# Optimization experiments

Hardware: AMD Instinct MI355X
Metric: run time of the kernel (lower is better)

Reference implementation:

```python
import jax, jax.numpy as jnp
import numpy as np

N = 10000      # nodes
E = 160000     # edges (before self-loops)
IN = 256
NEG_SLOPE = 0.2  # PyG GATConv default


def gat_layer(x, src, dst, W, a_src, a_dst, bias, heads, concat, n):
    # x: [n, in_dim]; W: [in_dim, heads*C]; a_src/a_dst: [heads, C]
    C = W.shape[1] // heads
    h = (x @ W).reshape(n, heads, C)                      # [n,H,C]
    es = jnp.einsum('nhc,hc->nh', h, a_src)               # [n,H]
    ed = jnp.einsum('nhc,hc->nh', h, a_dst)               # [n,H]
    e = jax.nn.leaky_relu(es[src] + ed[dst], NEG_SLOPE)   # [E,H]
    # segment softmax over destination node (every node has a self-loop)
    emax = jax.ops.segment_max(e, dst, num_segments=n)    # [n,H]
    al = jnp.exp(e - emax[dst])                           # [E,H]
    den = jax.ops.segment_sum(al, dst, num_segments=n)    # [n,H]
    al = al / den[dst]
    out = jax.ops.segment_sum(h[src] * al[:, :, None], dst, num_segments=n)  # [n,H,C]
    out = out.reshape(n, heads * C) if concat else out.mean(axis=1)
    return out + bias


def setup_inputs() -> dict:
    key = jax.random.key(0)
    ks = jax.random.split(key, 16)
    s = 0.05
    p = lambda k, shp: jax.random.normal(k, shp, dtype=jnp.float32) * s
    return {
        'x': jax.random.normal(ks[0], (N, IN), dtype=jnp.float32),
        'edge_index': jax.random.randint(ks[1], (2, E), 0, N, dtype=jnp.int64),
        'proj_w': p(ks[2], (IN, 512)), 'proj_b': jnp.zeros((512,), jnp.float32),
        'w1': p(ks[3], (512, 4 * 512)),  'as1': p(ks[4], (4, 512)), 'ad1': p(ks[5], (4, 512)),  'b1': jnp.zeros((2048,), jnp.float32),
        'w2': p(ks[6], (2048, 4 * 512)), 'as2': p(ks[7], (4, 512)), 'ad2': p(ks[8], (4, 512)),  'b2': jnp.zeros((2048,), jnp.float32),
        'w3': p(ks[9], (2048, 2 * 512)), 'as3': p(ks[10], (2, 512)), 'ad3': p(ks[11], (2, 512)), 'b3': jnp.zeros((512,), jnp.float32),
    }


def reference(x, edge_index, proj_w, proj_b, w1, as1, ad1, b1,
              w2, as2, ad2, b2, w3, as3, ad3, b3):
    n = x.shape[0]
    loops = jnp.arange(n, dtype=edge_index.dtype)
    src = jnp.concatenate([edge_index[0], loops])   # PyG add_self_loops=True
    dst = jnp.concatenate([edge_index[1], loops])
    h = x @ proj_w + proj_b                         # dropout is identity in eval
    h = gat_layer(h, src, dst, w1, as1, ad1, b1, 4, True, n)
    h = jax.nn.elu(h)
    h = gat_layer(h, src, dst, w2, as2, ad2, b2, 4, True, n)
    h = jax.nn.elu(h)
    h = gat_layer(h, src, dst, w3, as3, ad3, b3, 2, False, n)
    return h
```

## Files before the change

### kernel.cpp

```cpp
#include <hip/hip_runtime.h>
#include <hip/hip_bf16.h>
#include <math.h>

#define CDIV(a,b) (((a)+(b)-1)/(b))

typedef __bf16  bf16x8 __attribute__((ext_vector_type(8)));
typedef float   f32x4  __attribute__((ext_vector_type(4)));
typedef unsigned short u16x8 __attribute__((ext_vector_type(8)));
typedef unsigned short u16x4 __attribute__((ext_vector_type(4)));

__device__ __forceinline__ float bf2f(unsigned short u) {
    union { unsigned int i; float f; } x; x.i = ((unsigned int)u) << 16; return x.f;
}
__device__ __forceinline__ unsigned short f2bf(float f) {
    union { float f; unsigned int i; } x; x.f = f;
    unsigned int r = x.i + 0x7fff + ((x.i >> 16) & 1);
    return (unsigned short)(r >> 16);
}

__global__ void hist_kernel(const int* __restrict__ ei, int* __restrict__ deg,
                            int E, int Et) {
    int e = blockIdx.x * blockDim.x + threadIdx.x;
    if (e >= Et) return;
    int d = (e < E) ? ei[E + e] : (e - E);
    atomicAdd(&deg[d], 1);
}

__global__ void scan_kernel(const int* __restrict__ deg, int* __restrict__ off, int n) {
    __shared__ int wsum[16];
    __shared__ int carry_s;
    int t = threadIdx.x, lane = t & 63, wv = t >> 6;
    if (t == 0) carry_s = 0;
    __syncthreads();
    for (int base = 0; base < n; base += 1024) {
        int v = (base + t < n) ? deg[base + t] : 0;
        int x = v;
#pragma unroll
        for (int o = 1; o < 64; o <<= 1) {
            int y = __shfl_up(x, o);
            if (lane >= o) x += y;
        }
        if (lane == 63) wsum[wv] = x;
        __syncthreads();
        if (wv == 0 && lane < 16) {
            int s = wsum[lane];
#pragma unroll
            for (int o = 1; o < 16; o <<= 1) {
                int y = __shfl_up(s, o);
                if (lane >= o) s += y;
            }
            wsum[lane] = s;
        }
        __syncthreads();
        int wprev = (wv == 0) ? 0 : wsum[wv - 1];
        int incl = carry_s + wprev + x;
        if (base + t < n) off[base + t] = incl - v;
        __syncthreads();
        if (t == 1023) carry_s = incl;
        __syncthreads();
    }
    if (t == 0) off[n] = carry_s;
}

__global__ void scatter_kernel(const int* __restrict__ ei, const int* __restrict__ off,
                               int* __restrict__ cur, int* __restrict__ csr,
                               int E, int Et) {
    int e = blockIdx.x * blockDim.x + threadIdx.x;
    if (e >= Et) return;
    int s, d;
    if (e < E) { s = ei[e]; d = ei[E + e]; } else { s = e - E; d = s; }
    int pos = off[d] + atomicAdd(&cur[d], 1);
    csr[pos] = s;
}

__global__ void prep_t_kernel(const float* __restrict__ wa, __hip_bfloat16* __restrict__ wta,
                              const float* __restrict__ wb, __hip_bfloat16* __restrict__ wtb,
                              const float* __restrict__ wc, __hip_bfloat16* __restrict__ wtc,
                              int t0, int t1, int t2) {
    __shared__ float tile[32][33];
    int bid = blockIdx.x;
    const float* w; __hip_bfloat16* wt; int K, N, r;
    if (bid < t0)      { w = wa; wt = wta; K = 512;  N = 2048; r = bid; }
    else if (bid < t1) { w = wb; wt = wtb; K = 2048; N = 2048; r = bid - t0; }
    else               { w = wc; wt = wtc; K = 2048; N = 1024; r = bid - t1; }
    (void)t2;
    int kt = K >> 5;
    int kb = (r % kt) * 32, nb = (r / kt) * 32;
    int tx = threadIdx.x & 31, ty = threadIdx.x >> 5;
    for (int i = ty; i < 32; i += 8)
        tile[i][tx] = w[(size_t)(kb + i) * N + nb + tx];
    __syncthreads();
    for (int i = ty; i < 32; i += 8)
        wt[(size_t)(nb + i) * K + kb + tx] = __float2bfloat16(tile[tx][i]);
}

__global__ void cvt2_kernel(const float* __restrict__ a, __hip_bfloat16* __restrict__ ao,
                            int na4,
                            const float* __restrict__ b, __hip_bfloat16* __restrict__ bo,
                            int nb4) {
    int i = blockIdx.x * blockDim.x + threadIdx.x;
    const float* src; __hip_bfloat16* dst; int idx;
    if (i < na4) { src = a; dst = ao; idx = i * 4; }
    else if (i < na4 + nb4) { src = b; dst = bo; idx = (i - na4) * 4; }
    else return;
    float4 v = *(const float4*)(src + idx);
    dst[idx + 0] = __float2bfloat16(v.x);
    dst[idx + 1] = __float2bfloat16(v.y);
    dst[idx + 2] = __float2bfloat16(v.z);
    dst[idx + 3] = __float2bfloat16(v.w);
}

__global__ void beff_kernel(const float* __restrict__ pb, const float* __restrict__ w1,
                            float* __restrict__ beff, int N) {
    int j  = blockIdx.x * 256 + threadIdx.x;
    int k0 = blockIdx.y * 64;
    float s = 0.f;
#pragma unroll
    for (int k = 0; k < 64; k++)
        s = fmaf(pb[k0 + k], w1[(size_t)(k0 + k) * N + j], s);
    atomicAdd(&beff[j], s);
}

__global__ void va_kernel(const __hip_bfloat16* __restrict__ w_efft,
                          const float* __restrict__ b_eff,
                          const float* __restrict__ as1, const float* __restrict__ ad1,
                          const float* __restrict__ b1,
                          float* __restrict__ va, float* __restrict__ cvec,
                          float* __restrict__ b1s) {
    int j = blockIdx.x, t = threadIdx.x;
    if (j == 8) {
        for (int i = t; i < 2048; i += 256) b1s[i] = b_eff[i] + b1[i];
        return;
    }
    int h = j & 3;
    const float* a = ((j < 4) ? as1 : ad1) + h * 512;
    __shared__ float aLDS[512];
    __shared__ float red[256];
    for (int c = t; c < 512; c += 256) aLDS[c] = a[c];
    __syncthreads();
    float acc = 0.f;
    const unsigned short* wb = (const unsigned short*)w_efft + (size_t)h * 512 * 256 + t;
    for (int c = 0; c < 512; c++)
        acc = fmaf(aLDS[c], bf2f(wb[(size_t)c * 256]), acc);
    va[j * 256 + t] = acc;
    float cp = b_eff[h * 512 + t] * aLDS[t] + b_eff[h * 512 + 256 + t] * aLDS[256 + t];
    red[t] = cp;
    __syncthreads();
    for (int s = 128; s > 0; s >>= 1) {
        if (t < s) red[t] += red[t + s];
        __syncthreads();
    }
    if (t == 0) cvec[j] = red[0];
}

__global__ void es1_kernel(const __hip_bfloat16* __restrict__ x_bf,
                           const float* __restrict__ va, const float* __restrict__ cvec,
                           float* __restrict__ es, float* __restrict__ ed) {
    int node = blockIdx.x, l = threadIdx.x;
    u16x4 xv = *(const u16x4*)((const unsigned short*)x_bf + (size_t)node * 256 + l * 4);
    float xf[4];
#pragma unroll
    for (int k = 0; k < 4; k++) xf[k] = bf2f(xv[k]);
    float dot[8];
#pragma unroll
    for (int j = 0; j < 8; j++) {
        float4 v = *(const float4*)(va + j * 256 + l * 4);
        dot[j] = xf[0] * v.x + xf[1] * v.y + xf[2] * v.z + xf[3] * v.w;
    }
#pragma unroll
    for (int j = 0; j < 8; j++)
        for (int o = 32; o; o >>= 1) dot[j] += __shfl_down(dot[j], o);
    if (l == 0) {
#pragma unroll
        for (int h = 0; h < 4; h++) {
            es[node * 4 + h] = dot[h] + cvec[h];
            ed[node * 4 + h] = dot[4 + h] + cvec[4 + h];
        }
    }
}

__global__ __launch_bounds__(256) void agg1x_kernel(
    const __hip_bfloat16* __restrict__ x_bf, const float* __restrict__ es,
    const float* __restrict__ ed, const int* __restrict__ csr,
    const int* __restrict__ off, __hip_bfloat16* __restrict__ z)
{
    __shared__ float alds[64][4];
    __shared__ int   slds[64];
    int d = blockIdx.x, t = threadIdx.x;
    int beg = off[d], end = off[d + 1];
    float acc[4] = {0.f, 0.f, 0.f, 0.f}, den[4] = {0.f, 0.f, 0.f, 0.f};
    float edd[4];
#pragma unroll
    for (int h = 0; h < 4; h++) edd[h] = ed[d * 4 + h];
    const unsigned short* xb = (const unsigned short*)x_bf;

    for (int cb = beg; cb < end; cb += 64) {
        int cl = end - cb; if (cl > 64) cl = 64;
        int i = t >> 2, h = t & 3;
        if (i < cl) {
            int s = csr[cb + i];
            if (h == 0) slds[i] = s;
            float e = es[s * 4 + h] + edd[h];
            e = (e > 0.f) ? e : 0.2f * e;
            alds[i][h] = __expf(e);
        }
        __syncthreads();
        for (int ii = 0; ii < cl; ii++) {
            int s = slds[ii];
            float xv = bf2f(xb[(size_t)s * 256 + t]);
#pragma unroll
            for (int hh = 0; hh < 4; hh++) {
                float a = alds[ii][hh];
                den[hh] += a;
                acc[hh] = fmaf(a, xv, acc[hh]);
            }
        }
        __syncthreads();
    }
    unsigned short* zb = (unsigned short*)z + (size_t)d * 1024;
#pragma unroll
    for (int h = 0; h < 4; h++)
        zb[h * 256 + t] = f2bf(acc[h] / den[h]);
}

__device__ __forceinline__ void gload16(void* lds, const void* g) {
    __builtin_amdgcn_global_load_lds(
        (const __attribute__((address_space(1))) void*)g,
        (__attribute__((address_space(3))) void*)lds, 16, 0, 0);
}

__global__ __launch_bounds__(256) void gemm_bf16_kernel(
    const __hip_bfloat16* __restrict__ A,
    const __hip_bfloat16* __restrict__ BT,
    const float* __restrict__ bias,
    __hip_bfloat16* __restrict__ Cb,
    int M, int N, int K, int lda, int hko, int do_elu,
    int MB, int NB, int XT, int NBH)
{
    __shared__ __align__(16) __hip_bfloat16 As[128 * 32];
    __shared__ __align__(16) __hip_bfloat16 Bs[128 * 32];

    const int bid  = blockIdx.x;
    const int xcd  = bid & 7;
    const int slot = bid >> 3;
    const int per_yh = XT * NBH;
    const int yh    = slot / per_yh;
    const int rem   = slot - yh * per_yh;
    const int x_sub = rem / NBH;
    const int ys    = rem - x_sub * NBH;
    const int yb    = yh * NBH + ys;
    const int xb    = xcd * XT + x_sub;
    if (xb >= MB || yb >= NB) return;

    const int tid = threadIdx.x;
    const int m0 = xb * 128, n0 = yb * 128;
    const int w = tid >> 6, l = tid & 63;
    const int wm = (w & 1) * 64, wn = (w >> 1) * 64;
    const int lm = l & 15, lq = l >> 4;

    f32x4 acc[4][4] = {};

    const int arow = tid >> 2;
    const int acol = (tid & 3) * 8;
    const __hip_bfloat16* Ag = A + (size_t)(m0 + arow) * lda + acol + (n0 >> 9) * hko;
    const __hip_bfloat16* Bg = BT + (size_t)(n0 + arow) * K + acol;
    char* AsW = (char*)As + (w << 10);
    char* BsW = (char*)Bs + (w << 10);

    for (int k0 = 0; k0 < K; k0 += 32) {
        gload16(AsW,        Ag + k0);
        gload16(AsW + 4096, Ag + (size_t)64 * lda + k0);
        gload16(BsW,        Bg + k0);
        gload16(BsW + 4096, Bg + (size_t)64 * K + k0);
        __syncthreads();
        bf16x8 af[4], bfr[4];
#pragma unroll
        for (int i = 0; i < 4; i++)
            af[i] = *(const bf16x8*)(As + (wm + i * 16 + lm) * 32 + lq * 8);
#pragma unroll
        for (int j = 0; j < 4; j++)
            bfr[j] = *(const bf16x8*)(Bs + (wn + j * 16 + lm) * 32 + lq * 8);
#pragma unroll
        for (int i = 0; i < 4; i++)
#pragma unroll
            for (int j = 0; j < 4; j++)
                acc[i][j] = __builtin_amdgcn_mfma_f32_16x16x32_bf16(
                    af[i], bfr[j], acc[i][j], 0, 0, 0);
        __syncthreads();
    }

#pragma unroll
    for (int i = 0; i < 4; i++) {
        int rb = m0 + wm + i * 16 + lq * 4;
#pragma unroll
        for (int r = 0; r < 4; r++) {
            int row = rb + r;
            if (row >= M) continue;
#pragma unroll
            for (int j = 0; j < 4; j++) {
                int col = n0 + wn + j * 16 + lm;
                float v = acc[i][j][r];
                if (bias) v += bias[col];
                if (do_elu) v = (v > 0.f) ? v : expm1f(v);
                Cb[(size_t)row * N + col] = __float2bfloat16(v);
            }
        }
    }
}

__global__ __launch_bounds__(512, 2) void gemm256_kernel(
    const __hip_bfloat16* __restrict__ A,
    const __hip_bfloat16* __restrict__ BT,
    __hip_bfloat16* __restrict__ Cb,
    int M, int N, int K, int MT, int nfull)
{
    __shared__ __align__(16) char smem[131072];
    const int NT = K >> 6;

    const int cpx  = gridDim.x >> 3;
    const int bid  = blockIdx.x;
    const int slot = (bid & 7) * cpx + (bid >> 3);
    int mt, ntl;
    if (slot < nfull) { mt = slot % MT; ntl = slot / MT; }
    else              { ntl = nfull / MT; mt = (nfull % MT) + (slot - nfull); }
    const int m0 = mt << 8, n0 = ntl << 8;

    const int tid = threadIdx.x;
    const int w  = tid >> 6, l = tid & 63;
    const int wr = w >> 2, wc = w & 3;
    const int lm = l & 15, lq = l >> 4;

    const int srow = tid >> 3;
    const int scol = ((l & 7) << 3) ^ ((l >> 3) << 3);
    const __hip_bfloat16* As0 = A  + (size_t)(m0 + srow) * K + scol;
    const __hip_bfloat16* Bs0 = BT + (size_t)(n0 + srow) * K + scol;
    const size_t rs64  = (size_t)64  * K;
    const size_t rs128 = (size_t)128 * K;
    char* const stA = smem +          ((size_t)w << 10);
    char* const stB = smem + 65536 +  ((size_t)w << 10);

    auto STAGE_A = [&](int par, int hf, int tt) {
        char* d = stA + (((par << 1) | hf) << 14);
        const __hip_bfloat16* s = As0 + (size_t)hf * rs128 + (tt << 6);
        gload16(d,        s);
        gload16(d + 8192, s + rs64);
    };
    auto STAGE_B = [&](int par, int hf, int tt) {
        char* d = stB + (((par << 1) | hf) << 14);
        const __hip_bfloat16* s = Bs0 + (size_t)hf * rs128 + (tt << 6);
        gload16(d,        s);
        gload16(d + 8192, s + rs64);
    };

    const int roff = lm << 7;
    const int xm   = (lm & 7) << 4;
    const int off0 = (lq << 4) ^ xm;
    const int off1 = off0 ^ 64;
    const int bsel = 65536 + ((wc & 1) << 13);

    f32x4  acc[8][4] = {};
    bf16x8 af[8][2];
    bf16x8 bfr[2][2];

    STAGE_A(0, 0, 0); STAGE_A(0, 1, 0);
    STAGE_B(0, 0, 0); STAGE_B(0, 1, 0);
    STAGE_A(1, 0, 1); STAGE_A(1, 1, 1);
    asm volatile("s_waitcnt vmcnt(4)" ::: "memory");
    __builtin_amdgcn_s_barrier();

    for (int t = 0; t < NT; ++t) {
        const int par = t & 1;
        const char* aS = smem + (((par << 1) | wr)        << 14) + roff;
        const char* bS = smem + (((par << 1) | (wc >> 1)) << 14) + bsel + roff;

#pragma unroll
        for (int i = 0; i < 4; ++i) {
            af[i][0] = *(const bf16x8*)(aS + i * 2048 + off0);
            af[i][1] = *(const bf16x8*)(aS + i * 2048 + off1);
        }
#pragma unroll
        for (int j = 0; j < 2; ++j) {
            bfr[j][0] = *(const bf16x8*)(bS + j * 2048 + off0);
            bfr[j][1] = *(const bf16x8*)(bS + j * 2048 + off1);
        }
        if (t + 1 < NT) STAGE_B(par ^ 1, 0, t + 1);
        __builtin_amdgcn_s_barrier();
        asm volatile("s_waitcnt lgkmcnt(0)" ::: "memory");
        __builtin_amdgcn_sched_barrier(0);
        __builtin_amdgcn_s_setprio(1);
#pragma unroll
        for (int i = 0; i < 4; ++i)
#pragma unroll
            for (int j = 0; j < 2; ++j) {
                acc[i][j] = __builtin_amdgcn_mfma_f32_16x16x32_bf16(af[i][0], bfr[j][0], acc[i][j], 0, 0, 0);
                acc[i][j] = __builtin_amdgcn_mfma_f32_16x16x32_bf16(af[i][1], bfr[j][1], acc[i][j], 0, 0, 0);
            }
        __builtin_amdgcn_s_setprio(0);
        __builtin_amdgcn_s_barrier();

#pragma unroll
        for (int i = 4; i < 8; ++i) {
            af[i][0] = *(const bf16x8*)(aS + i * 2048 + off0);
            af[i][1] = *(const bf16x8*)(aS + i * 2048 + off1);
        }
        if (t + 1 < NT) STAGE_B(par ^ 1, 1, t + 1);
        __builtin_amdgcn_s_barrier();
        asm volatile("s_waitcnt lgkmcnt(0)" ::: "memory");
        __builtin_amdgcn_sched_barrier(0);
        __builtin_amdgcn_s_setprio(1);
#pragma unroll
        for (int i = 4; i < 8; ++i)
#pragma unroll
            for (int j = 0; j < 2; ++j) {
                acc[i][j] = __builtin_amdgcn_mfma_f32_16x16x32_bf16(af[i][0], bfr[j][0], acc[i][j], 0, 0, 0);
                acc[i][j] = __builtin_amdgcn_mfma_f32_16x16x32_bf16(af[i][1], bfr[j][1], acc[i][j], 0, 0, 0);
            }
        __builtin_amdgcn_s_setprio(0);
        __builtin_amdgcn_s_barrier();

#pragma unroll
        for (int j = 0; j < 2; ++j) {
            bfr[j][0] = *(const bf16x8*)(bS + (j + 2) * 2048 + off0);
            bfr[j][1] = *(const bf16x8*)(bS + (j + 2) * 2048 + off1);
        }
        if (t + 2 < NT) STAGE_A(par, 0, t + 2);
        __builtin_amdgcn_s_barrier();
        asm volatile("s_waitcnt lgkmcnt(0)" ::: "memory");
        __builtin_amdgcn_sched_barrier(0);
        __builtin_amdgcn_s_setprio(1);
#pragma unroll
        for (int i = 0; i < 4; ++i)
#pragma unroll
            for (int j = 0; j < 2; ++j) {
                acc[i][j + 2] = __builtin_amdgcn_mfma_f32_16x16x32_bf16(af[i][0], bfr[j][0], acc[i][j + 2], 0, 0, 0);
                acc[i][j + 2] = __builtin_amdgcn_mfma_f32_16x16x32_bf16(af[i][1], bfr[j][1], acc[i][j + 2], 0, 0, 0);
            }
        __builtin_amdgcn_s_setprio(0);
        __builtin_amdgcn_s_barrier();

        if (t + 2 < NT) STAGE_A(par, 1, t + 2);
        __builtin_amdgcn_s_barrier();
        __builtin_amdgcn_sched_barrier(0);
        __builtin_amdgcn_s_setprio(1);
#pragma unroll
        for (int i = 4; i < 8; ++i)
#pragma unroll
            for (int j = 0; j < 2; ++j) {
                acc[i][j + 2] = __builtin_amdgcn_mfma_f32_16x16x32_bf16(af[i][0], bfr[j][0], acc[i][j + 2], 0, 0, 0);
                acc[i][j + 2] = __builtin_amdgcn_mfma_f32_16x16x32_bf16(af[i][1], bfr[j][1], acc[i][j + 2], 0, 0, 0);
            }
        __builtin_amdgcn_s_setprio(0);
        if (t + 2 < NT)      { asm volatile("s_waitcnt vmcnt(4)" ::: "memory"); }
        else if (t + 1 < NT) { asm volatile("s_waitcnt vmcnt(0)" ::: "memory"); }
        __builtin_amdgcn_s_barrier();
    }

#pragma unroll
    for (int i = 0; i < 8; ++i) {
        int rb = m0 + wr * 128 + i * 16 + lq * 4;
#pragma unroll
        for (int r = 0; r < 4; ++r) {
            int row = rb + r;
            if (row >= M) continue;
#pragma unroll
            for (int j = 0; j < 4; ++j) {
                int col = n0 + wc * 64 + j * 16 + lm;
                Cb[(size_t)row * N + col] = __float2bfloat16(acc[i][j][r]);
            }
        }
    }
}

__global__ __launch_bounds__(256, 2) void gemm128_kernel(
    const __hip_bfloat16* __restrict__ A,
    const __hip_bfloat16* __restrict__ BT,
    __hip_bfloat16* __restrict__ Cb,
    int M, int N, int K, int mode, int RT)
{
    __shared__ __align__(16) char smem[65536];
    const int NT = K >> 6;

    const int cpx  = gridDim.x >> 3;
    const int bid  = blockIdx.x;
    const int slot = (bid & 7) * cpx + (bid >> 3);
    int r, c;
    if (mode == 0) { r = slot % RT; c = slot / RT; }
    else {
        if (slot < 96) { c = 12 + slot / 48; r = 32 + slot % 48; }
        else           { int u = slot - 96; c = 14 + u / 80; r = u % 80; }
    }
    const int m0 = r << 7, n0 = c << 7;

    const int tid = threadIdx.x;
    const int w = tid >> 6, l = tid & 63;
    const int wm = (w & 1) << 6, wn = (w >> 1) << 6;
    const int lm = l & 15, lq = l >> 4;

    const int srow = tid >> 3;
    const int scol = (((tid & 7) ^ ((tid >> 3) & 7)) << 3);
    const __hip_bfloat16* Ag = A  + (size_t)(m0 + srow) * K + scol;
    const __hip_bfloat16* Bg = BT + (size_t)(n0 + srow) * K + scol;
    const size_t rs32 = (size_t)32 * K;
    char* const dA = smem +         ((size_t)w << 10);
    char* const dB = smem + 16384 + ((size_t)w << 10);

    auto STAGE = [&](int par, int tt) {
        char* pa = dA + (par << 15);
        char* pb = dB + (par << 15);
        const __hip_bfloat16* sa = Ag + (tt << 6);
        const __hip_bfloat16* sb = Bg + (tt << 6);
#pragma unroll
        for (int s = 0; s < 4; ++s) {
            gload16(pa + (s << 12), sa + (size_t)s * rs32);
            gload16(pb + (s << 12), sb + (size_t)s * rs32);
        }
    };

    const int roff = lm << 7;
    const int off0 = (lq << 4) ^ ((lm & 7) << 4);
    const int off1 = off0 ^ 64;

    f32x4 acc[4][4] = {};

    STAGE(0, 0);
    asm volatile("s_waitcnt vmcnt(0)" ::: "memory");
    __builtin_amdgcn_s_barrier();

    for (int t = 0; t < NT; ++t) {
        const int par = t & 1;
        if (t + 1 < NT) STAGE(par ^ 1, t + 1);
        const char* aS = smem + (par << 15) +         wm * 128 + roff;
        const char* bS = smem + (par << 15) + 16384 + wn * 128 + roff;
        bf16x8 af[4][2], bfr[4][2];
#pragma unroll
        for (int i = 0; i < 4; ++i) {
            af[i][0]  = *(const bf16x8*)(aS + i * 2048 + off0);
            af[i][1]  = *(const bf16x8*)(aS + i * 2048 + off1);
            bfr[i][0] = *(const bf16x8*)(bS + i * 2048 + off0);
            bfr[i][1] = *(const bf16x8*)(bS + i * 2048 + off1);
        }
        asm volatile("s_waitcnt lgkmcnt(0)" ::: "memory");
        __builtin_amdgcn_sched_barrier(0);
        __builtin_amdgcn_s_setprio(1);
#pragma unroll
        for (int i = 0; i < 4; ++i)
#pragma unroll
            for (int j = 0; j < 4; ++j) {
                acc[i][j] = __builtin_amdgcn_mfma_f32_16x16x32_bf16(af[i][0], bfr[j][0], acc[i][j], 0, 0, 0);
                acc[i][j] = __builtin_amdgcn_mfma_f32_16x16x32_bf16(af[i][1], bfr[j][1], acc[i][j], 0, 0, 0);
            }
        __builtin_amdgcn_s_setprio(0);
        if (t + 1 < NT) asm volatile("s_waitcnt vmcnt(0)" ::: "memory");
        __builtin_amdgcn_s_barrier();
    }

#pragma unroll
    for (int i = 0; i < 4; ++i) {
        int rb = m0 + wm + i * 16 + lq * 4;
#pragma unroll
        for (int r2 = 0; r2 < 4; ++r2) {
            int row = rb + r2;
            if (row >= M) continue;
#pragma unroll
            for (int j = 0; j < 4; ++j) {
                int col = n0 + wn + j * 16 + lm;
                Cb[(size_t)row * N + col] = __float2bfloat16(acc[i][j][r2]);
            }
        }
    }
}

__global__ void esed_kernel(const __hip_bfloat16* __restrict__ h,
                            const float* __restrict__ a_src,
                            const float* __restrict__ a_dst,
                            float* __restrict__ es, float* __restrict__ ed, int H) {
    int nidx = blockIdx.x;
    int t = threadIdx.x;
    int head = t >> 6, lane = t & 63;
    const unsigned short* hp =
        (const unsigned short*)h + (size_t)nidx * H * 512 + head * 512 + lane * 8;
    const float* sp = a_src + head * 512 + lane * 8;
    const float* dp = a_dst + head * 512 + lane * 8;
    u16x8 hv = *(const u16x8*)hp;
    float4 s0 = *(const float4*)sp, s1 = *(const float4*)(sp + 4);
    float4 d0 = *(const float4*)dp, d1 = *(const float4*)(dp + 4);
    float hf[8];
#pragma unroll
    for (int k = 0; k < 8; k++) hf[k] = bf2f(hv[k]);
    float s = hf[0]*s0.x + hf[1]*s0.y + hf[2]*s0.z + hf[3]*s0.w
            + hf[4]*s1.x + hf[5]*s1.y + hf[6]*s1.z + hf[7]*s1.w;
    float d = hf[0]*d0.x + hf[1]*d0.y + hf[2]*d0.z + hf[3]*d0.w
            + hf[4]*d1.x + hf[5]*d1.y + hf[6]*d1.z + hf[7]*d1.w;
    for (int o = 32; o; o >>= 1) { s += __shfl_down(s, o); d += __shfl_down(d, o); }
    if (lane == 0) { es[nidx * H + head] = s; ed[nidx * H + head] = d; }
}

template<int H>
__global__ __launch_bounds__(256) void alpha_kernel(
    const float* __restrict__ es, const float* __restrict__ ed,
    const int* __restrict__ csr, const int* __restrict__ off,
    float* __restrict__ alpha, int n)
{
    int d = blockIdx.x * 4 + (threadIdx.x >> 6);
    if (d >= n) return;
    int lane = threadIdx.x & 63;
    int beg = off[d], end = off[d + 1];
    float edd[H], den[H];
#pragma unroll
    for (int h = 0; h < H; h++) { edd[h] = ed[d * H + h]; den[h] = 0.f; }
    for (int i = beg + lane; i < end; i += 64) {
        int s = csr[i];
#pragma unroll
        for (int h = 0; h < H; h++) {
            float e = es[s * H + h] + edd[h];
            e = (e > 0.f) ? e : 0.2f * e;
            den[h] += __expf(e);
        }
    }
#pragma unroll
    for (int h = 0; h < H; h++) {
        for (int o = 32; o; o >>= 1) den[h] += __shfl_down(den[h], o);
        den[h] = __shfl(den[h], 0);
        den[h] = 1.f / den[h];
    }
    for (int i = beg + lane; i < end; i += 64) {
        int s = csr[i];
#pragma unroll
        for (int h = 0; h < H; h++) {
            float e = es[s * H + h] + edd[h];
            e = (e > 0.f) ? e : 0.2f * e;
            alpha[(size_t)i * H + h] = __expf(e) * den[h];
        }
    }
}

__global__ __launch_bounds__(256) void agg2s_kernel(
    const __hip_bfloat16* __restrict__ h, const float* __restrict__ alpha,
    const int* __restrict__ csr, const int* __restrict__ off,
    const float* __restrict__ bias, __hip_bfloat16* __restrict__ outB, int n)
{
    const int bid   = blockIdx.x;
    const int slice = bid & 7;
    const int head  = slice >> 1;
    const int wvs   = (bid >> 3) * 4 + (threadIdx.x >> 6);
    const int lane  = threadIdx.x & 63;
    const int half  = lane >> 5;
    const int c0    = slice * 256 + (lane & 31) * 8;
    const unsigned short* hb = (const unsigned short*)h;
    float bv[8];
#pragma unroll
    for (int k = 0; k < 8; k++) bv[k] = bias[c0 + k];

    for (int d = wvs; d < n; d += 1024) {
        int beg = off[d], end = off[d + 1];
        float acc[8] = {0.f, 0.f, 0.f, 0.f, 0.f, 0.f, 0.f, 0.f};
        int i = beg + half;
        for (; i + 2 < end; i += 4) {
            int s0 = csr[i], s1 = csr[i + 2];
            float a0 = alpha[(size_t)i * 4 + head];
            float a1 = alpha[(size_t)(i + 2) * 4 + head];
            u16x8 v0 = *(const u16x8*)(hb + (size_t)s0 * 2048 + c0);
            u16x8 v1 = *(const u16x8*)(hb + (size_t)s1 * 2048 + c0);
#pragma unroll
            for (int k = 0; k < 8; k++) acc[k] = fmaf(a0, bf2f(v0[k]), acc[k]);
#pragma unroll
            for (int k = 0; k < 8; k++) acc[k] = fmaf(a1, bf2f(v1[k]), acc[k]);
        }
        for (; i < end; i += 2) {
            int s0 = csr[i];
            float a0 = alpha[(size_t)i * 4 + head];
            u16x8 v0 = *(const u16x8*)(hb + (size_t)s0 * 2048 + c0);
#pragma unroll
            for (int k = 0; k < 8; k++) acc[k] = fmaf(a0, bf2f(v0[k]), acc[k]);
        }
#pragma unroll
        for (int k = 0; k < 8; k++) acc[k] += __shfl_xor(acc[k], 32);
        if (half == 0) {
            u16x8 ov;
#pragma unroll
            for (int k = 0; k < 8; k++) {
                float v = acc[k] + bv[k];
                v = (v > 0.f) ? v : expm1f(v);
                ov[k] = f2bf(v);
            }
            *(u16x8*)((unsigned short*)outB + (size_t)d * 2048 + c0) = ov;
        }
    }
}

__global__ __launch_bounds__(256) void agg3s_kernel(
    const __hip_bfloat16* __restrict__ h, const float* __restrict__ alpha,
    const int* __restrict__ csr, const int* __restrict__ off,
    float* __restrict__ part, int n)
{
    const int bid   = blockIdx.x;
    const int xcd   = bid & 7;
    const int slice = xcd >> 1;
    const int head  = slice >> 1;
    const int sb    = ((bid >> 3) << 1) | (xcd & 1);
    const int wvs   = sb * 4 + (threadIdx.x >> 6);
    const int lane  = threadIdx.x & 63;
    const int half  = lane >> 5;
    const int c0    = slice * 256 + (lane & 31) * 8;
    const unsigned short* hb = (const unsigned short*)h;

    for (int d = wvs; d < n; d += 2048) {
        int beg = off[d], end = off[d + 1];
        float acc[8] = {0.f, 0.f, 0.f, 0.f, 0.f, 0.f, 0.f, 0.f};
        int i = beg + half;
        for (; i + 2 < end; i += 4) {
            int s0 = csr[i], s1 = csr[i + 2];
            float a0 = alpha[(size_t)i * 2 + head];
            float a1 = alpha[(size_t)(i + 2) * 2 + head];
            u16x8 v0 = *(const u16x8*)(hb + (size_t)s0 * 1024 + c0);
            u16x8 v1 = *(const u16x8*)(hb + (size_t)s1 * 1024 + c0);
#pragma unroll
            for (int k = 0; k < 8; k++) acc[k] = fmaf(a0, bf2f(v0[k]), acc[k]);
#pragma unroll
            for (int k = 0; k < 8; k++) acc[k] = fmaf(a1, bf2f(v1[k]), acc[k]);
        }
        for (; i < end; i += 2) {
            int s0 = csr[i];
            float a0 = alpha[(size_t)i * 2 + head];
            u16x8 v0 = *(const u16x8*)(hb + (size_t)s0 * 1024 + c0);
#pragma unroll
            for (int k = 0; k < 8; k++) acc[k] = fmaf(a0, bf2f(v0[k]), acc[k]);
        }
#pragma unroll
        for (int k = 0; k < 8; k++) acc[k] += __shfl_xor(acc[k], 32);
        if (half == 0) {
            float* pp = part + (size_t)d * 1024 + c0;
            *(float4*)pp       = make_float4(acc[0], acc[1], acc[2], acc[3]);
            *(float4*)(pp + 4) = make_float4(acc[4], acc[5], acc[6], acc[7]);
        }
    }
}

__global__ void comb3_kernel(const float* __restrict__ part,
                             const float* __restrict__ b3,
                             float* __restrict__ out, int n) {
    int idx = blockIdx.x * 256 + threadIdx.x;
    if (idx >= n * 128) return;
    int d = idx >> 7, c = (idx & 127) * 4;
    float4 p0 = *(const float4*)(part + (size_t)d * 1024 + c);
    float4 p1 = *(const float4*)(part + (size_t)d * 1024 + 512 + c);
    float4 bb = *(const float4*)(b3 + c);
    float4 o;
    o.x = 0.5f * (p0.x + p1.x) + bb.x;
    o.y = 0.5f * (p0.y + p1.y) + bb.y;
    o.z = 0.5f * (p0.z + p1.z) + bb.z;
    o.w = 0.5f * (p0.w + p1.w) + bb.w;
    *(float4*)(out + (size_t)d * 512 + c) = o;
}

extern "C" void kernel_launch(void* const* d_in, const int* in_sizes, int n_in,
                              void* d_out, int out_size, void* d_ws, size_t ws_size,
                              hipStream_t stream) {
    const float* x      = (const float*)d_in[0];
    const int*   ei     = (const int*)  d_in[1];
    const float* proj_w = (const float*)d_in[2];
    const float* proj_b = (const float*)d_in[3];
    const float* w1  = (const float*)d_in[4];
    const float* as1 = (const float*)d_in[5];
    const float* ad1 = (const float*)d_in[6];
    const float* b1  = (const float*)d_in[7];
    const float* w2  = (const float*)d_in[8];
    const float* as2 = (const float*)d_in[9];
    const float* ad2 = (const float*)d_in[10];
    const float* b2  = (const float*)d_in[11];
    const float* w3  = (const float*)d_in[12];
    const float* as3 = (const float*)d_in[13];
    const float* ad3 = (const float*)d_in[14];
    const float* b3  = (const float*)d_in[15];

    const int n    = in_sizes[0] / 256;
    const int E    = in_sizes[1] / 2;
    const int Et   = E + n;
    const int MB   = CDIV(n, 128);
    const int MB2  = CDIV(n, 256);
    const int Mpad = MB2 * 256;
    const int XT   = CDIV(MB, 8);

    char* p = (char*)d_ws;
    auto carve = [&](size_t bytes) {
        void* r = (void*)p;
        p += (bytes + 255) & ~(size_t)255;
        return r;
    };
    __hip_bfloat16* h_bf    = (__hip_bfloat16*)carve((size_t)Mpad * 2048 * sizeof(__hip_bfloat16));
    __hip_bfloat16* act_bf  = (__hip_bfloat16*)carve((size_t)Mpad * 2048 * sizeof(__hip_bfloat16));
    __hip_bfloat16* x_bf    = (__hip_bfloat16*)carve((size_t)Mpad * 256 * sizeof(__hip_bfloat16));
    __hip_bfloat16* pw_bf   = (__hip_bfloat16*)carve((size_t)256 * 512 * sizeof(__hip_bfloat16));
    __hip_bfloat16* w1t     = (__hip_bfloat16*)carve((size_t)2048 * 512 * sizeof(__hip_bfloat16));
    __hip_bfloat16* w2t     = (__hip_bfloat16*)carve((size_t)2048 * 2048 * sizeof(__hip_bfloat16));
    __hip_bfloat16* w3t     = (__hip_bfloat16*)carve((size_t)1024 * 2048 * sizeof(__hip_bfloat16));
    __hip_bfloat16* w_efft  = (__hip_bfloat16*)carve((size_t)2048 * 256 * sizeof(__hip_bfloat16));
    float* b_eff = (float*)carve((size_t)2048 * sizeof(float));
    float* b1s   = (float*)carve((size_t)2048 * sizeof(float));
    float* va    = (float*)carve((size_t)8 * 256 * sizeof(float));
    float* cvec  = (float*)carve((size_t)8 * sizeof(float));
    float* es  = (float*)carve((size_t)n * 4 * sizeof(float));
    float* ed  = (float*)carve((size_t)n * 4 * sizeof(float));
    float* alpha = (float*)carve((size_t)Et * 4 * sizeof(float));
    int* deg = (int*)carve((size_t)2 * n * sizeof(int));
    int* cur = deg + n;
    int* off = (int*)carve((size_t)(n + 1) * sizeof(int));
    int* csr = (int*)carve((size_t)Et * sizeof(int));
    __hip_bfloat16* z_bf = h_bf;
    float* part = (float*)act_bf;
    (void)ws_size; (void)n_in;

    hipMemsetAsync(deg, 0, 2 * n * sizeof(int), stream);
    hipMemsetAsync(b_eff, 0, 2048 * sizeof(float), stream);
    hist_kernel<<<CDIV(Et, 256), 256, 0, stream>>>(ei, deg, E, Et);
    scan_kernel<<<1, 1024, 0, stream>>>(deg, off, n);
    scatter_kernel<<<CDIV(Et, 256), 256, 0, stream>>>(ei, off, cur, csr, E, Et);

    const int t0 = (512 / 32) * (2048 / 32);
    const int t1 = t0 + (2048 / 32) * (2048 / 32);
    const int t2 = t1 + (2048 / 32) * (1024 / 32);
    prep_t_kernel<<<t2, 256, 0, stream>>>(w1, w1t, w2, w2t, w3, w3t, t0, t1, t2);
    const int na4 = 256 * 512 / 4, nb4 = n * 256 / 4;
    cvt2_kernel<<<CDIV(na4 + nb4, 256), 256, 0, stream>>>(proj_w, pw_bf, na4, x, x_bf, nb4);

    gemm_bf16_kernel<<<8 * 2 * 2, 256, 0, stream>>>(
        w1t, pw_bf, nullptr, w_efft, 2048, 256, 512, 512, 0, 0, 16, 2, 2, 2);
    beff_kernel<<<dim3(2048 / 256, 512 / 64), 256, 0, stream>>>(proj_b, w1, b_eff, 2048);

    va_kernel<<<9, 256, 0, stream>>>(w_efft, b_eff, as1, ad1, b1, va, cvec, b1s);

    es1_kernel<<<n, 64, 0, stream>>>(x_bf, va, cvec, es, ed);
    agg1x_kernel<<<n, 256, 0, stream>>>(x_bf, es, ed, csr, off, z_bf);
    gemm_bf16_kernel<<<8 * XT * 16, 256, 0, stream>>>(
        z_bf, w_efft, b1s, act_bf, n, 2048, 256, 1024, 256, 1, MB, 16, XT, 16);

    gemm256_kernel<<<256, 512, 0, stream>>>(act_bf, w2t, h_bf, n, 2048, 2048, 40, 240);
    gemm128_kernel<<<256, 256, 0, stream>>>(act_bf, w2t, h_bf, n, 2048, 2048, 1, 0);
    esed_kernel<<<n, 4 * 64, 0, stream>>>(h_bf, as2, ad2, es, ed, 4);
    alpha_kernel<4><<<CDIV(n, 4), 256, 0, stream>>>(es, ed, csr, off, alpha, n);
    agg2s_kernel<<<2048, 256, 0, stream>>>(h_bf, alpha, csr, off, b2, act_bf, n);

    gemm128_kernel<<<640, 256, 0, stream>>>(act_bf, w3t, h_bf, n, 1024, 2048, 0, 80);
    esed_kernel<<<n, 2 * 64, 0, stream>>>(h_bf, as3, ad3, es, ed, 2);
    alpha_kernel<2><<<CDIV(n, 4), 256, 0, stream>>>(es, ed, csr, off, alpha, n);
    agg3s_kernel<<<2048, 256, 0, stream>>>(h_bf, alpha, csr, off, part, n);
    comb3_kernel<<<CDIV(n * 128, 256), 256, 0, stream>>>(part, b3, (float*)d_out, n);
}
```

Before: 579.7 us.

## Pack source byte offset with alpha per edge-head; fuse layer-3 head mean via atomics

The alpha kernel now writes an interleaved record per edge and head holding the precomputed byte offset of the source row together with the attention weight. The aggregation kernels then need one 8-byte load instead of separate csr and alpha loads and an address multiply. Layer 3 drops the partial buffer and combine kernel: the output is pre-filled with the bias and each head atomically adds half its contribution. In exchange the record array is larger than the old alpha array, and the float atomic adds make the head summation order nondeterministic.

```diff
diff --git a/kernel.cpp b/kernel.cpp
--- a/kernel.cpp
+++ b/kernel.cpp
@@ -595,11 +595,11 @@
     if (lane == 0) { es[nidx * H + head] = s; ed[nidx * H + head] = d; }
 }
 
-template<int H>
-__global__ __launch_bounds__(256) void alpha_kernel(
+template<int H, int SHIFT>
+__global__ __launch_bounds__(256) void alpharec_kernel(
     const float* __restrict__ es, const float* __restrict__ ed,
     const int* __restrict__ csr, const int* __restrict__ off,
-    float* __restrict__ alpha, int n)
+    uint2* __restrict__ rec, int n)
 {
     int d = blockIdx.x * 4 + (threadIdx.x >> 6);
     if (d >= n) return;
@@ -625,19 +625,21 @@
     }
     for (int i = beg + lane; i < end; i += 64) {
         int s = csr[i];
+        unsigned obytes = ((unsigned)s) << SHIFT;
 #pragma unroll
         for (int h = 0; h < H; h++) {
             float e = es[s * H + h] + edd[h];
             e = (e > 0.f) ? e : 0.2f * e;
-            alpha[(size_t)i * H + h] = __expf(e) * den[h];
+            float a = __expf(e) * den[h];
+            rec[(size_t)i * H + h] = make_uint2(obytes, __float_as_uint(a));
         }
     }
 }
 
 __global__ __launch_bounds__(256) void agg2s_kernel(
-    const __hip_bfloat16* __restrict__ h, const float* __restrict__ alpha,
-    const int* __restrict__ csr, const int* __restrict__ off,
-    const float* __restrict__ bias, __hip_bfloat16* __restrict__ outB, int n)
+    const __hip_bfloat16* __restrict__ h, const uint2* __restrict__ rec,
+    const int* __restrict__ off, const float* __restrict__ bias,
+    __hip_bfloat16* __restrict__ outB, int n)
 {
     const int bid   = blockIdx.x;
     const int slice = bid & 7;
@@ -646,7 +648,8 @@
     const int lane  = threadIdx.x & 63;
     const int half  = lane >> 5;
     const int c0    = slice * 256 + (lane & 31) * 8;
-    const unsigned short* hb = (const unsigned short*)h;
+    const unsigned c0b = (unsigned)c0 * 2;
+    const char* hb = (const char*)h;
     float bv[8];
 #pragma unroll
     for (int k = 0; k < 8; k++) bv[k] = bias[c0 + k];
@@ -656,20 +659,21 @@
         float acc[8] = {0.f, 0.f, 0.f, 0.f, 0.f, 0.f, 0.f, 0.f};
         int i = beg + half;
         for (; i + 2 < end; i += 4) {
-            int s0 = csr[i], s1 = csr[i + 2];
-            float a0 = alpha[(size_t)i * 4 + head];
-            float a1 = alpha[(size_t)(i + 2) * 4 + head];
-            u16x8 v0 = *(const u16x8*)(hb + (size_t)s0 * 2048 + c0);
-            u16x8 v1 = *(const u16x8*)(hb + (size_t)s1 * 2048 + c0);
+            uint2 r0 = rec[i * 4 + head];
+            uint2 r1 = rec[(i + 2) * 4 + head];
+            u16x8 v0 = *(const u16x8*)(hb + (size_t)(r0.x + c0b));
+            u16x8 v1 = *(const u16x8*)(hb + (size_t)(r1.x + c0b));
+            float a0 = __uint_as_float(r0.y);
+            float a1 = __uint_as_float(r1.y);
 #pragma unroll
             for (int k = 0; k < 8; k++) acc[k] = fmaf(a0, bf2f(v0[k]), acc[k]);
 #pragma unroll
             for (int k = 0; k < 8; k++) acc[k] = fmaf(a1, bf2f(v1[k]), acc[k]);
         }
         for (; i < end; i += 2) {
-            int s0 = csr[i];
-            float a0 = alpha[(size_t)i * 4 + head];
-            u16x8 v0 = *(const u16x8*)(hb + (size_t)s0 * 2048 + c0);
+            uint2 r0 = rec[i * 4 + head];
+            u16x8 v0 = *(const u16x8*)(hb + (size_t)(r0.x + c0b));
+            float a0 = __uint_as_float(r0.y);
 #pragma unroll
             for (int k = 0; k < 8; k++) acc[k] = fmaf(a0, bf2f(v0[k]), acc[k]);
         }
@@ -689,9 +693,8 @@
 }
 
 __global__ __launch_bounds__(256) void agg3s_kernel(
-    const __hip_bfloat16* __restrict__ h, const float* __restrict__ alpha,
-    const int* __restrict__ csr, const int* __restrict__ off,
-    float* __restrict__ part, int n)
+    const __hip_bfloat16* __restrict__ h, const uint2* __restrict__ rec,
+    const int* __restrict__ off, float* __restrict__ out, int n)
 {
     const int bid   = blockIdx.x;
     const int xcd   = bid & 7;
@@ -702,55 +705,50 @@
     const int lane  = threadIdx.x & 63;
     const int half  = lane >> 5;
     const int c0    = slice * 256 + (lane & 31) * 8;
-    const unsigned short* hb = (const unsigned short*)h;
+    const unsigned c0b = (unsigned)c0 * 2;
+    const int outc  = c0 & 511;
+    const char* hb = (const char*)h;
 
     for (int d = wvs; d < n; d += 2048) {
         int beg = off[d], end = off[d + 1];
         float acc[8] = {0.f, 0.f, 0.f, 0.f, 0.f, 0.f, 0.f, 0.f};
         int i = beg + half;
         for (; i + 2 < end; i += 4) {
-            int s0 = csr[i], s1 = csr[i + 2];
-            float a0 = alpha[(size_t)i * 2 + head];
-            float a1 = alpha[(size_t)(i + 2) * 2 + head];
-            u16x8 v0 = *(const u16x8*)(hb + (size_t)s0 * 1024 + c0);
-            u16x8 v1 = *(const u16x8*)(hb + (size_t)s1 * 1024 + c0);
+            uint2 r0 = rec[i * 2 + head];
+            uint2 r1 = rec[(i + 2) * 2 + head];
+            u16x8 v0 = *(const u16x8*)(hb + (size_t)(r0.x + c0b));
+            u16x8 v1 = *(const u16x8*)(hb + (size_t)(r1.x + c0b));
+            float a0 = __uint_as_float(r0.y);
+            float a1 = __uint_as_float(r1.y);
 #pragma unroll
             for (int k = 0; k < 8; k++) acc[k] = fmaf(a0, bf2f(v0[k]), acc[k]);
 #pragma unroll
             for (int k = 0; k < 8; k++) acc[k] = fmaf(a1, bf2f(v1[k]), acc[k]);
         }
         for (; i < end; i += 2) {
-            int s0 = csr[i];
-            float a0 = alpha[(size_t)i * 2 + head];
-            u16x8 v0 = *(const u16x8*)(hb + (size_t)s0 * 1024 + c0);
+            uint2 r0 = rec[i * 2 + head];
+            u16x8 v0 = *(const u16x8*)(hb + (size_t)(r0.x + c0b));
+            float a0 = __uint_as_float(r0.y);
 #pragma unroll
             for (int k = 0; k < 8; k++) acc[k] = fmaf(a0, bf2f(v0[k]), acc[k]);
         }
 #pragma unroll
         for (int k = 0; k < 8; k++) acc[k] += __shfl_xor(acc[k], 32);
         if (half == 0) {
-            float* pp = part + (size_t)d * 1024 + c0;
-            *(float4*)pp       = make_float4(acc[0], acc[1], acc[2], acc[3]);
-            *(float4*)(pp + 4) = make_float4(acc[4], acc[5], acc[6], acc[7]);
-        }
-    }
-}
-
-__global__ void comb3_kernel(const float* __restrict__ part,
-                             const float* __restrict__ b3,
+            float* op = out + (size_t)d * 512 + outc;
+#pragma unroll
+            for (int k = 0; k < 8; k++)
+                atomicAdd(op + k, 0.5f * acc[k]);
+        }
+    }
+}
+
+__global__ void fillb_kernel(const float* __restrict__ b3,
                              float* __restrict__ out, int n) {
     int idx = blockIdx.x * 256 + threadIdx.x;
     if (idx >= n * 128) return;
     int d = idx >> 7, c = (idx & 127) * 4;
-    float4 p0 = *(const float4*)(part + (size_t)d * 1024 + c);
-    float4 p1 = *(const float4*)(part + (size_t)d * 1024 + 512 + c);
-    float4 bb = *(const float4*)(b3 + c);
-    float4 o;
-    o.x = 0.5f * (p0.x + p1.x) + bb.x;
-    o.y = 0.5f * (p0.y + p1.y) + bb.y;
-    o.z = 0.5f * (p0.z + p1.z) + bb.z;
-    o.w = 0.5f * (p0.w + p1.w) + bb.w;
-    *(float4*)(out + (size_t)d * 512 + c) = o;
+    *(float4*)(out + (size_t)d * 512 + c) = *(const float4*)(b3 + c);
 }
 
 extern "C" void kernel_launch(void* const* d_in, const int* in_sizes, int n_in,
@@ -801,13 +799,12 @@
     float* cvec  = (float*)carve((size_t)8 * sizeof(float));
     float* es  = (float*)carve((size_t)n * 4 * sizeof(float));
     float* ed  = (float*)carve((size_t)n * 4 * sizeof(float));
-    float* alpha = (float*)carve((size_t)Et * 4 * sizeof(float));
+    uint2* rec = (uint2*)carve((size_t)Et * 4 * sizeof(uint2));
     int* deg = (int*)carve((size_t)2 * n * sizeof(int));
     int* cur = deg + n;
     int* off = (int*)carve((size_t)(n + 1) * sizeof(int));
     int* csr = (int*)carve((size_t)Et * sizeof(int));
     __hip_bfloat16* z_bf = h_bf;
-    float* part = (float*)act_bf;
     (void)ws_size; (void)n_in;
 
     hipMemsetAsync(deg, 0, 2 * n * sizeof(int), stream);
@@ -837,12 +834,12 @@
     gemm256_kernel<<<256, 512, 0, stream>>>(act_bf, w2t, h_bf, n, 2048, 2048, 40, 240);
     gemm128_kernel<<<256, 256, 0, stream>>>(act_bf, w2t, h_bf, n, 2048, 2048, 1, 0);
     esed_kernel<<<n, 4 * 64, 0, stream>>>(h_bf, as2, ad2, es, ed, 4);
-    alpha_kernel<4><<<CDIV(n, 4), 256, 0, stream>>>(es, ed, csr, off, alpha, n);
-    agg2s_kernel<<<2048, 256, 0, stream>>>(h_bf, alpha, csr, off, b2, act_bf, n);
+    alpharec_kernel<4, 12><<<CDIV(n, 4), 256, 0, stream>>>(es, ed, csr, off, rec, n);
+    agg2s_kernel<<<2048, 256, 0, stream>>>(h_bf, rec, off, b2, act_bf, n);
 
     gemm128_kernel<<<640, 256, 0, stream>>>(act_bf, w3t, h_bf, n, 1024, 2048, 0, 80);
     esed_kernel<<<n, 2 * 64, 0, stream>>>(h_bf, as3, ad3, es, ed, 2);
-    alpha_kernel<2><<<CDIV(n, 4), 256, 0, stream>>>(es, ed, csr, off, alpha, n);
-    agg3s_kernel<<<2048, 256, 0, stream>>>(h_bf, alpha, csr, off, part, n);
-    comb3_kernel<<<CDIV(n * 128, 256), 256, 0, stream>>>(part, b3, (float*)d_out, n);
-}
+    alpharec_kernel<2, 11><<<CDIV(n, 4), 256, 0, stream>>>(es, ed, csr, off, rec, n);
+    fillb_kernel<<<CDIV(n * 128, 256), 256, 0, stream>>>(b3, (float*)d_out, n);
+    agg3s_kernel<<<2048, 256, 0, stream>>>(h_bf, rec, off, (float*)d_out, n);
+}
```

Result: slower. 852.5 us (+47.1%).
